# Optimization experiments

Hardware: AMD Instinct MI355X
Metric: run time of the kernel (lower is better)

The kernel has to match this reference:

```python
import jax, jax.numpy as jnp
import numpy as np


def _gru_cell(x, h, W_ih, W_hh, b_ih, b_hh):
    # PyTorch GRUCell math, gate order (r, z, n) along the 3*H axis.
    gi = x @ W_ih.T + b_ih          # [B, 3H]
    gh = h @ W_hh.T + b_hh          # [B, 3H]
    i_r, i_z, i_n = jnp.split(gi, 3, axis=-1)
    h_r, h_z, h_n = jnp.split(gh, 3, axis=-1)
    r = jax.nn.sigmoid(i_r + h_r)
    z = jax.nn.sigmoid(i_z + h_z)
    n = jnp.tanh(i_n + r * h_n)
    return (1.0 - z) * n + z * h


def setup_inputs() -> dict:
    key = jax.random.key(0)
    ks = jax.random.split(key, 12)
    V, E, H, L, B, T = 16000, 512, 1024, 2, 32, 64
    s = 0.05  # small init scale to keep gates unsaturated
    return {
        "hidden": jax.random.normal(ks[0], (L, B, H), jnp.float32),
        "embed": jax.random.normal(ks[1], (V, E), jnp.float32) * s,
        "W_ih0": jax.random.normal(ks[2], (3 * H, E), jnp.float32) * s,
        "W_hh0": jax.random.normal(ks[3], (3 * H, H), jnp.float32) * s,
        "b_ih0": jax.random.normal(ks[4], (3 * H,), jnp.float32) * s,
        "b_hh0": jax.random.normal(ks[5], (3 * H,), jnp.float32) * s,
        "W_ih1": jax.random.normal(ks[6], (3 * H, H), jnp.float32) * s,
        "W_hh1": jax.random.normal(ks[7], (3 * H, H), jnp.float32) * s,
        "b_ih1": jax.random.normal(ks[8], (3 * H,), jnp.float32) * s,
        "b_hh1": jax.random.normal(ks[9], (3 * H,), jnp.float32) * s,
        "W_out": jax.random.normal(ks[10], (V, H), jnp.float32) * s,
        "b_out": jax.random.normal(ks[11], (V,), jnp.float32) * s,
        "max_len": 64,
        "batch_size": 32,
    }


def reference(hidden, embed, W_ih0, W_hh0, b_ih0, b_hh0,
              W_ih1, W_hh1, b_ih1, b_hh1, W_out, b_out,
              max_len, batch_size):
    # target=None path: teacher_forcing_ratio forced to 0 -> greedy argmax decode.
    tok0 = jnp.zeros((batch_size,), jnp.int32)  # curr_token starts at zeros

    def step(carry, _):
        h, tok = carry                      # h: [2, B, H], tok: [B] int32
        x = embed[tok]                      # [B, E] embedding lookup
        h0 = _gru_cell(x, h[0], W_ih0, W_hh0, b_ih0, b_hh0)
        h1 = _gru_cell(h0, h[1], W_ih1, W_hh1, b_ih1, b_hh1)
        logits = h1 @ W_out.T + b_out       # [B, V]
        tok_next = jnp.argmax(logits, axis=1).astype(jnp.int32)
        return (jnp.stack([h0, h1]), tok_next), logits

    (_, _), outputs = jax.lax.scan(step, (hidden, tok0), None, length=max_len)
    return outputs  # [max_len, B, V]
```

## Files before the change

### kernel.cpp

```cpp
#include <hip/hip_runtime.h>
#include <stdint.h>

#define V_ 16000
#define E_ 512
#define H_ 1024
#define B_ 32
#define T_ 64
#define NG_ 3072
#define NR_ 6144
#define TPAD_ 8

typedef float f32x4 __attribute__((ext_vector_type(4)));
typedef unsigned long long u64;

__device__ __forceinline__ unsigned int fkey(float f) {
    unsigned int u = __float_as_uint(f);
    return (u & 0x80000000u) ? ~u : (u | 0x80000000u);
}

__global__ void init_kernel(const float* __restrict__ hidden,
                            float* __restrict__ h0, float* __restrict__ h1,
                            u64* __restrict__ tokpk) {
    int idx = blockIdx.x * blockDim.x + threadIdx.x;
    if (idx < B_ * H_) {
        h0[idx] = hidden[idx];
        h1[idx] = hidden[B_ * H_ + idx];
    }
    if (idx < T_ * B_ * TPAD_) tokpk[idx] = 0ull;
}

__device__ __forceinline__ void gemm_core64(
    const float* wq0, const float* wq1, const float* wq2, const float* wq3,
    const float* aq0, const float* aq1,
    int dW0, int dW1, int dW2, int dW3, int dA0, int dA1,
    int nch, float* lds, int tid, float acc[8][8])
{
    const int ks = tid >> 5, pos = tid & 31;
    const int rg = pos >> 2, bgp = pos & 3;

    f32x4 w0 = *(const f32x4*)wq0, w1 = *(const f32x4*)wq1;
    f32x4 w2 = *(const f32x4*)wq2, w3 = *(const f32x4*)wq3;
    f32x4 a0 = *(const f32x4*)aq0, a1 = *(const f32x4*)aq1;
    *(f32x4*)&lds[dW0] = w0; *(f32x4*)&lds[dW1] = w1;
    *(f32x4*)&lds[dW2] = w2; *(f32x4*)&lds[dW3] = w3;
    *(f32x4*)&lds[dA0] = a0; *(f32x4*)&lds[dA1] = a1;
    __syncthreads();

    int cur = 0;
    for (int c = 0; c < nch; c++) {
        if (c + 1 < nch) {
            const int o = (c + 1) << 6;
            w0 = *(const f32x4*)(wq0 + o); w1 = *(const f32x4*)(wq1 + o);
            w2 = *(const f32x4*)(wq2 + o); w3 = *(const f32x4*)(wq3 + o);
            a0 = *(const f32x4*)(aq0 + o); a1 = *(const f32x4*)(aq1 + o);
        }
        const float* Wb = &lds[cur * 6144];
        const float* Ab = Wb + 4096;
        #pragma unroll
        for (int kk = 0; kk < 2; kk++) {
            const int k4 = ks * 2 + kk;
            f32x4 ww[8], ha[8];
            #pragma unroll
            for (int vi = 0; vi < 8; vi++) {
                const int row = rg + 8 * vi;
                ww[vi] = *(const f32x4*)&Wb[(row << 6) + ((k4 ^ rg) << 2)];
            }
            #pragma unroll
            for (int j = 0; j < 8; j++) {
                const int br = bgp + 4 * j;
                ha[j] = *(const f32x4*)&Ab[(br << 6) + ((k4 ^ (br & 7)) << 2)];
            }
            #pragma unroll
            for (int vi = 0; vi < 8; vi++)
                #pragma unroll
                for (int j = 0; j < 8; j++)
                    acc[vi][j] += ww[vi].x*ha[j].x + ww[vi].y*ha[j].y
                                + ww[vi].z*ha[j].z + ww[vi].w*ha[j].w;
        }
        if (c + 1 < nch) {
            float* L = &lds[(cur ^ 1) * 6144];
            *(f32x4*)&L[dW0] = w0; *(f32x4*)&L[dW1] = w1;
            *(f32x4*)&L[dW2] = w2; *(f32x4*)&L[dW3] = w3;
            *(f32x4*)&L[dA0] = a0; *(f32x4*)&L[dA1] = a1;
        }
        __syncthreads();
        cur ^= 1;
    }
}

__device__ __forceinline__ void reduce_totl(float* lds, int tid, float acc[8][8])
{
    const int ks = tid >> 5, pos = tid & 31;
    {
        float* dst = &lds[(ks * 32 + pos) * 68];
        #pragma unroll
        for (int vi = 0; vi < 8; vi++) {
            f32x4 p0 = {acc[vi][0], acc[vi][1], acc[vi][2], acc[vi][3]};
            f32x4 p1 = {acc[vi][4], acc[vi][5], acc[vi][6], acc[vi][7]};
            *(f32x4*)&dst[vi * 8]     = p0;
            *(f32x4*)&dst[vi * 8 + 4] = p1;
        }
    }
    __syncthreads();
    const int vi2 = tid >> 5, pos2 = tid & 31;
    f32x4 s0 = {0.f, 0.f, 0.f, 0.f}, s1 = {0.f, 0.f, 0.f, 0.f};
    #pragma unroll
    for (int k = 0; k < 8; k++) {
        const float* src = &lds[(k * 32 + pos2) * 68 + vi2 * 8];
        s0 += *(const f32x4*)src;
        s1 += *(const f32x4*)(src + 4);
    }
    __syncthreads();
    const int row = (pos2 >> 2) + 8 * vi2;
    const int bb  = pos2 & 3;
    lds[(bb +  0) * 68 + row] = s0.x;
    lds[(bb +  4) * 68 + row] = s0.y;
    lds[(bb +  8) * 68 + row] = s0.z;
    lds[(bb + 12) * 68 + row] = s0.w;
    lds[(bb + 16) * 68 + row] = s1.x;
    lds[(bb + 20) * 68 + row] = s1.y;
    lds[(bb + 24) * 68 + row] = s1.z;
    lds[(bb + 28) * 68 + row] = s1.w;
    __syncthreads();
}

__global__ __launch_bounds__(256) void gemm_gru(
    const float* __restrict__ Wih, const float* __restrict__ Whh, int Kih,
    const float* __restrict__ xbase, int xld,
    const float* __restrict__ embed, const u64* __restrict__ tokprev,
    int t, int tmode,
    const float* __restrict__ hprev,
    float* __restrict__ gbuf)
{
    __shared__ float lds[17408];
    const int tid = threadIdx.x;
    const int blk0 = blockIdx.x;
    const int kslice = blk0 >= 96 ? 1 : 0;
    const int tile = blk0 - kslice * 96;
    const int k4s = tid & 15;
    const int rr  = tid >> 4;

    const float* Wbase; int K, n0, nout;
    const float *ar0, *ar1;
    if (tile < 48) {
        n0 = tile * 64; nout = n0; Wbase = Wih; K = Kih;
        if (tmode) {
            int tok0 = 0, tok1 = 0;
            if (t > 0) {
                tok0 = (int)(0xFFFFFFFFu -
                       (unsigned)(tokprev[(size_t)rr * TPAD_] & 0xFFFFFFFFull));
                tok1 = (int)(0xFFFFFFFFu -
                       (unsigned)(tokprev[(size_t)(rr + 16) * TPAD_] & 0xFFFFFFFFull));
            }
            ar0 = embed + (size_t)tok0 * Kih;
            ar1 = embed + (size_t)tok1 * Kih;
        } else {
            ar0 = xbase + (size_t)rr * xld;
            ar1 = xbase + (size_t)(rr + 16) * xld;
        }
    } else {
        n0 = (tile - 48) * 64; nout = NG_ + n0; Wbase = Whh; K = H_;
        ar0 = hprev + (size_t)rr * H_;
        ar1 = hprev + (size_t)(rr + 16) * H_;
    }
    const int koff = kslice * (K >> 1);
    const int nch  = K >> 7;

    const float *wq0, *wq1, *wq2, *wq3;
    int dW0, dW1, dW2, dW3;
    {
        const int r0 = rr, r1 = 16 + rr, r2 = 32 + rr, r3 = 48 + rr;
        wq0 = Wbase + (size_t)(n0 + r0) * K + koff + k4s * 4;
        wq1 = Wbase + (size_t)(n0 + r1) * K + koff + k4s * 4;
        wq2 = Wbase + (size_t)(n0 + r2) * K + koff + k4s * 4;
        wq3 = Wbase + (size_t)(n0 + r3) * K + koff + k4s * 4;
        dW0 = (r0 << 6) + ((k4s ^ (r0 & 7)) << 2);
        dW1 = (r1 << 6) + ((k4s ^ (r1 & 7)) << 2);
        dW2 = (r2 << 6) + ((k4s ^ (r2 & 7)) << 2);
        dW3 = (r3 << 6) + ((k4s ^ (r3 & 7)) << 2);
    }
    const float* aq0 = ar0 + koff + k4s * 4;
    const float* aq1 = ar1 + koff + k4s * 4;
    const int dA0 = 4096 + (rr << 6) + ((k4s ^ (rr & 7)) << 2);
    const int dA1 = 4096 + ((rr + 16) << 6) + ((k4s ^ (rr & 7)) << 2);

    float acc[8][8] = {};
    gemm_core64(wq0, wq1, wq2, wq3, aq0, aq1,
                dW0, dW1, dW2, dW3, dA0, dA1, nch, lds, tid, acc);
    reduce_totl(lds, tid, acc);

    {
        const int b = tid >> 3, seg = tid & 7;
        float* gout = gbuf + (size_t)kslice * B_ * NR_
                    + (size_t)b * NR_ + nout + seg * 8;
        f32x4 x0 = *(f32x4*)&lds[b * 68 + seg * 8];
        f32x4 x1 = *(f32x4*)&lds[b * 68 + seg * 8 + 4];
        *(f32x4*)gout = x0;
        *(f32x4*)(gout + 4) = x1;
    }
}

__global__ __launch_bounds__(256) void combine_kernel(
    const float* __restrict__ gbuf,
    const float* __restrict__ bih, const float* __restrict__ bhh,
    const float* __restrict__ hprev, float* __restrict__ hnew)
{
    const int idx = blockIdx.x * 256 + threadIdx.x;
    const int b = idx >> 10, i = idx & 1023;
    const float* gb0 = gbuf + (size_t)b * NR_;
    const float* gb1 = gbuf + (size_t)(B_ + b) * NR_;
    const float gir = gb0[i]         + gb1[i];
    const float giz = gb0[H_ + i]    + gb1[H_ + i];
    const float gin = gb0[2*H_ + i]  + gb1[2*H_ + i];
    const float ghr = gb0[NG_ + i]        + gb1[NG_ + i];
    const float ghz = gb0[NG_ + H_ + i]   + gb1[NG_ + H_ + i];
    const float ghn = gb0[NG_ + 2*H_ + i] + gb1[NG_ + 2*H_ + i];
    const float Sr = gir + ghr + bih[i] + bhh[i];
    const float Sz = giz + ghz + bih[H_ + i] + bhh[H_ + i];
    const float rr = 1.f / (1.f + expf(-Sr));
    const float zz = 1.f / (1.f + expf(-Sz));
    const float nn = tanhf(gin + bih[2*H_ + i] + rr * (ghn + bhh[2*H_ + i]));
    const float hp = hprev[(size_t)b * H_ + i];
    hnew[(size_t)b * H_ + i] = (1.f - zz) * nn + zz * hp;
}

__global__ __launch_bounds__(256) void logits_kernel(
    const float* __restrict__ h1, const float* __restrict__ Wout,
    const float* __restrict__ bout, float* __restrict__ out_t,
    u64* __restrict__ tokpk_t)
{
    __shared__ float lds[17408];
    const int tid = threadIdx.x;
    const int v0 = blockIdx.x * 64;
    const int k4s = tid & 15;
    const int rr  = tid >> 4;

    const float *wq0, *wq1, *wq2, *wq3;
    int dW0, dW1, dW2, dW3;
    {
        const int r0 = rr, r1 = 16 + rr, r2 = 32 + rr, r3 = 48 + rr;
        wq0 = Wout + (size_t)(v0 + r0) * H_ + k4s * 4;
        wq1 = Wout + (size_t)(v0 + r1) * H_ + k4s * 4;
        wq2 = Wout + (size_t)(v0 + r2) * H_ + k4s * 4;
        wq3 = Wout + (size_t)(v0 + r3) * H_ + k4s * 4;
        dW0 = (r0 << 6) + ((k4s ^ (r0 & 7)) << 2);
        dW1 = (r1 << 6) + ((k4s ^ (r1 & 7)) << 2);
        dW2 = (r2 << 6) + ((k4s ^ (r2 & 7)) << 2);
        dW3 = (r3 << 6) + ((k4s ^ (r3 & 7)) << 2);
    }
    const float* aq0 = h1 + (size_t)rr * H_ + k4s * 4;
    const float* aq1 = h1 + (size_t)(rr + 16) * H_ + k4s * 4;
    const int dA0 = 4096 + (rr << 6) + ((k4s ^ (rr & 7)) << 2);
    const int dA1 = 4096 + ((rr + 16) << 6) + ((k4s ^ (rr & 7)) << 2);

    float acc[8][8] = {};
    gemm_core64(wq0, wq1, wq2, wq3, aq0, aq1,
                dW0, dW1, dW2, dW3, dA0, dA1, H_ >> 6, lds, tid, acc);
    reduce_totl(lds, tid, acc);

    u64* am = (u64*)(lds + 2176);
    {
        const int b = tid >> 3, seg = tid & 7;
        f32x4 x0 = *(f32x4*)&lds[b * 68 + seg * 8];
        f32x4 x1 = *(f32x4*)&lds[b * 68 + seg * 8 + 4];
        f32x4 bo0 = *(const f32x4*)(bout + v0 + seg * 8);
        f32x4 bo1 = *(const f32x4*)(bout + v0 + seg * 8 + 4);
        x0 += bo0; x1 += bo1;
        __builtin_nontemporal_store(
            x0, (f32x4*)(out_t + (size_t)b * V_ + v0 + seg * 8));
        __builtin_nontemporal_store(
            x1, (f32x4*)(out_t + (size_t)b * V_ + v0 + seg * 8 + 4));
        const int vb = v0 + seg * 8;
        float vals[8] = {x0.x, x0.y, x0.z, x0.w, x1.x, x1.y, x1.z, x1.w};
        u64 best = 0ull;
        #pragma unroll
        for (int i = 0; i < 8; i++) {
            u64 p = ((u64)fkey(vals[i]) << 32)
                  | (u64)(0xFFFFFFFFu - (unsigned)(vb + i));
            best = p > best ? p : best;
        }
        am[b * 8 + seg] = best;
    }
    __syncthreads();
    if (tid < 32) {
        u64 best = 0ull;
        #pragma unroll
        for (int q = 0; q < 8; q++) {
            u64 p = am[tid * 8 + q];
            best = p > best ? p : best;
        }
        atomicMax(&tokpk_t[(size_t)tid * TPAD_], best);
    }
}

extern "C" void kernel_launch(void* const* d_in, const int* in_sizes, int n_in,
                              void* d_out, int out_size, void* d_ws, size_t ws_size,
                              hipStream_t stream) {
    const float* hidden = (const float*)d_in[0];
    const float* embed  = (const float*)d_in[1];
    const float* Wih0   = (const float*)d_in[2];
    const float* Whh0   = (const float*)d_in[3];
    const float* bih0   = (const float*)d_in[4];
    const float* bhh0   = (const float*)d_in[5];
    const float* Wih1   = (const float*)d_in[6];
    const float* Whh1   = (const float*)d_in[7];
    const float* bih1   = (const float*)d_in[8];
    const float* bhh1   = (const float*)d_in[9];
    const float* Wout   = (const float*)d_in[10];
    const float* bout   = (const float*)d_in[11];
    float* out = (float*)d_out;

    const int BH = B_ * H_;
    float* ws = (float*)d_ws;
    float* h0buf = ws;
    float* h1buf = ws + 2 * BH;
    float* gbuf  = ws + 4 * BH;
    u64* tokpk = (u64*)(ws + 4 * BH + 2 * B_ * NR_);

    init_kernel<<<128, 256, 0, stream>>>(hidden, h0buf, h1buf, tokpk);

    for (int t = 0; t < T_; t++) {
        const int rp = t & 1, wp = (t + 1) & 1;
        const u64* tokprev = tokpk + (size_t)(t > 0 ? t - 1 : 0) * B_ * TPAD_;

        gemm_gru<<<192, 256, 0, stream>>>(
            Wih0, Whh0, E_, nullptr, 0, embed, tokprev, t, 1,
            h0buf + (size_t)rp * BH, gbuf);
        combine_kernel<<<128, 256, 0, stream>>>(
            gbuf, bih0, bhh0, h0buf + (size_t)rp * BH, h0buf + (size_t)wp * BH);

        gemm_gru<<<192, 256, 0, stream>>>(
            Wih1, Whh1, H_, h0buf + (size_t)wp * BH, H_, embed, tokprev, 0,
            0, h1buf + (size_t)rp * BH, gbuf);
        combine_kernel<<<128, 256, 0, stream>>>(
            gbuf, bih1, bhh1, h1buf + (size_t)rp * BH, h1buf + (size_t)wp * BH);

        logits_kernel<<<250, 256, 0, stream>>>(
            h1buf + (size_t)wp * BH, Wout, bout,
            out + (size_t)t * B_ * V_, tokpk + (size_t)t * B_ * TPAD_);
    }
}
```

Before: 3.944 ms.

## Fuse GRU combine into gemm kernel via grid-wide atomic barrier

```diff
diff --git a/kernel.cpp b/kernel.cpp
--- a/kernel.cpp
+++ b/kernel.cpp
@@ -9,6 +9,7 @@
 #define NG_ 3072
 #define NR_ 6144
 #define TPAD_ 8
+#define GGRID_ 192
 
 typedef float f32x4 __attribute__((ext_vector_type(4)));
 typedef unsigned long long u64;
@@ -18,15 +19,28 @@
     return (u & 0x80000000u) ? ~u : (u | 0x80000000u);
 }
 
+__device__ __forceinline__ float ld_cohf(const float* p) {
+    return __hip_atomic_load(p, __ATOMIC_RELAXED, __HIP_MEMORY_SCOPE_AGENT);
+}
+__device__ __forceinline__ void st_cohx4(float* p, f32x4 v) {
+    union { u64 q[2]; f32x4 v; } u;
+    u.v = v;
+    __hip_atomic_store((u64*)p,       u.q[0], __ATOMIC_RELAXED,
+                       __HIP_MEMORY_SCOPE_AGENT);
+    __hip_atomic_store(((u64*)p) + 1, u.q[1], __ATOMIC_RELAXED,
+                       __HIP_MEMORY_SCOPE_AGENT);
+}
+
 __global__ void init_kernel(const float* __restrict__ hidden,
                             float* __restrict__ h0, float* __restrict__ h1,
-                            u64* __restrict__ tokpk) {
+                            u64* __restrict__ tokpk, unsigned* __restrict__ cnt) {
     int idx = blockIdx.x * blockDim.x + threadIdx.x;
     if (idx < B_ * H_) {
         h0[idx] = hidden[idx];
         h1[idx] = hidden[B_ * H_ + idx];
     }
     if (idx < T_ * B_ * TPAD_) tokpk[idx] = 0ull;
+    if (idx < 32) cnt[idx] = 0u;
 }
 
 __device__ __forceinline__ void gemm_core64(
@@ -130,7 +144,10 @@
     const float* __restrict__ embed, const u64* __restrict__ tokprev,
     int t, int tmode,
     const float* __restrict__ hprev,
-    float* __restrict__ gbuf)
+    float* __restrict__ gbuf,
+    const float* __restrict__ bih, const float* __restrict__ bhh,
+    float* __restrict__ hnew,
+    unsigned* __restrict__ cnt, unsigned kseq)
 {
     __shared__ float lds[17408];
     const int tid = threadIdx.x;
@@ -195,33 +212,42 @@
                     + (size_t)b * NR_ + nout + seg * 8;
         f32x4 x0 = *(f32x4*)&lds[b * 68 + seg * 8];
         f32x4 x1 = *(f32x4*)&lds[b * 68 + seg * 8 + 4];
-        *(f32x4*)gout = x0;
-        *(f32x4*)(gout + 4) = x1;
-    }
-}
-
-__global__ __launch_bounds__(256) void combine_kernel(
-    const float* __restrict__ gbuf,
-    const float* __restrict__ bih, const float* __restrict__ bhh,
-    const float* __restrict__ hprev, float* __restrict__ hnew)
-{
-    const int idx = blockIdx.x * 256 + threadIdx.x;
-    const int b = idx >> 10, i = idx & 1023;
-    const float* gb0 = gbuf + (size_t)b * NR_;
-    const float* gb1 = gbuf + (size_t)(B_ + b) * NR_;
-    const float gir = gb0[i]         + gb1[i];
-    const float giz = gb0[H_ + i]    + gb1[H_ + i];
-    const float gin = gb0[2*H_ + i]  + gb1[2*H_ + i];
-    const float ghr = gb0[NG_ + i]        + gb1[NG_ + i];
-    const float ghz = gb0[NG_ + H_ + i]   + gb1[NG_ + H_ + i];
-    const float ghn = gb0[NG_ + 2*H_ + i] + gb1[NG_ + 2*H_ + i];
-    const float Sr = gir + ghr + bih[i] + bhh[i];
-    const float Sz = giz + ghz + bih[H_ + i] + bhh[H_ + i];
-    const float rr = 1.f / (1.f + expf(-Sr));
-    const float zz = 1.f / (1.f + expf(-Sz));
-    const float nn = tanhf(gin + bih[2*H_ + i] + rr * (ghn + bhh[2*H_ + i]));
-    const float hp = hprev[(size_t)b * H_ + i];
-    hnew[(size_t)b * H_ + i] = (1.f - zz) * nn + zz * hp;
+        st_cohx4(gout, x0);
+        st_cohx4(gout + 4, x1);
+    }
+    __syncthreads();
+
+    if (tid == 0) {
+        __hip_atomic_fetch_add(cnt, 1u, __ATOMIC_RELAXED,
+                               __HIP_MEMORY_SCOPE_AGENT);
+        const unsigned target = kseq * (unsigned)GGRID_;
+        while (__hip_atomic_load(cnt, __ATOMIC_RELAXED,
+                                 __HIP_MEMORY_SCOPE_AGENT) < target)
+            __builtin_amdgcn_s_sleep(2);
+    }
+    __syncthreads();
+
+    {
+        const int idx = blk0 * 256 + tid;
+        if (idx < B_ * H_) {
+            const int b = idx >> 10, i = idx & 1023;
+            const float* gb0 = gbuf + (size_t)b * NR_;
+            const float* gb1 = gbuf + (size_t)(B_ + b) * NR_;
+            const float gir = ld_cohf(gb0 + i)              + ld_cohf(gb1 + i);
+            const float giz = ld_cohf(gb0 + H_ + i)         + ld_cohf(gb1 + H_ + i);
+            const float gin = ld_cohf(gb0 + 2*H_ + i)       + ld_cohf(gb1 + 2*H_ + i);
+            const float ghr = ld_cohf(gb0 + NG_ + i)        + ld_cohf(gb1 + NG_ + i);
+            const float ghz = ld_cohf(gb0 + NG_ + H_ + i)   + ld_cohf(gb1 + NG_ + H_ + i);
+            const float ghn = ld_cohf(gb0 + NG_ + 2*H_ + i) + ld_cohf(gb1 + NG_ + 2*H_ + i);
+            const float Sr = gir + ghr + bih[i] + bhh[i];
+            const float Sz = giz + ghz + bih[H_ + i] + bhh[H_ + i];
+            const float rv = 1.f / (1.f + expf(-Sr));
+            const float zv = 1.f / (1.f + expf(-Sz));
+            const float nv = tanhf(gin + bih[2*H_ + i] + rv * (ghn + bhh[2*H_ + i]));
+            const float hp = hprev[(size_t)b * H_ + i];
+            hnew[(size_t)b * H_ + i] = (1.f - zv) * nv + zv * hp;
+        }
+    }
 }
 
 __global__ __launch_bounds__(256) void logits_kernel(
@@ -316,24 +342,25 @@
     float* h1buf = ws + 2 * BH;
     float* gbuf  = ws + 4 * BH;
     u64* tokpk = (u64*)(ws + 4 * BH + 2 * B_ * NR_);
-
-    init_kernel<<<128, 256, 0, stream>>>(hidden, h0buf, h1buf, tokpk);
+    unsigned* cnt = (unsigned*)(tokpk + (size_t)T_ * B_ * TPAD_);
+
+    init_kernel<<<128, 256, 0, stream>>>(hidden, h0buf, h1buf, tokpk, cnt);
 
     for (int t = 0; t < T_; t++) {
         const int rp = t & 1, wp = (t + 1) & 1;
         const u64* tokprev = tokpk + (size_t)(t > 0 ? t - 1 : 0) * B_ * TPAD_;
 
-        gemm_gru<<<192, 256, 0, stream>>>(
+        gemm_gru<<<GGRID_, 256, 0, stream>>>(
             Wih0, Whh0, E_, nullptr, 0, embed, tokprev, t, 1,
-            h0buf + (size_t)rp * BH, gbuf);
-        combine_kernel<<<128, 256, 0, stream>>>(
-            gbuf, bih0, bhh0, h0buf + (size_t)rp * BH, h0buf + (size_t)wp * BH);
-
-        gemm_gru<<<192, 256, 0, stream>>>(
+            h0buf + (size_t)rp * BH, gbuf,
+            bih0, bhh0, h0buf + (size_t)wp * BH,
+            cnt, (unsigned)(2 * t + 1));
+
+        gemm_gru<<<GGRID_, 256, 0, stream>>>(
             Wih1, Whh1, H_, h0buf + (size_t)wp * BH, H_, embed, tokprev, 0,
-            0, h1buf + (size_t)rp * BH, gbuf);
-        combine_kernel<<<128, 256, 0, stream>>>(
-            gbuf, bih1, bhh1, h1buf + (size_t)rp * BH, h1buf + (size_t)wp * BH);
+            0, h1buf + (size_t)rp * BH, gbuf,
+            bih1, bhh1, h1buf + (size_t)wp * BH,
+            cnt, (unsigned)(2 * t + 2));
 
         logits_kernel<<<250, 256, 0, stream>>>(
             h1buf + (size_t)wp * BH, Wout, bout,
```

Result: slower. 4.648 ms (+17.9%).
